# Kernel optimization log

Measured on AMD Instinct MI355X. Metric: run time of the kernel, lower is better.

## Reference

```python
import jax, jax.numpy as jnp
import numpy as np

D, H, N, T, B = 32, 128, 128, 256, 64   # input_dim, n_units, N_units, time_depth, batch
HEADS, THR, SHORT = 4, 0.01, 2
HD = H // HEADS


def setup_inputs() -> dict:
    key = jax.random.key(0)
    ks = iter(jax.random.split(key, 64))
    rn = lambda *s: jax.random.normal(next(ks), s, dtype=jnp.float32) * 0.1
    inp = {"x": jax.random.normal(next(ks), (B, T, D), dtype=jnp.float32)}
    for n_ in ["U_j", "U_i", "U_f", "U_o"]:
        inp[n_] = rn(D, 1, H)
    for n_ in ["W_j", "W_i", "W_f", "W_o"]:
        inp[n_] = rn(D, H, H)
    for n_ in ["B_j", "B_i", "B_f", "B_o"]:
        inp[n_] = jnp.full((D, H), 0.01, dtype=jnp.float32)
    for n_ in ["u_j", "u_i", "u_f", "u_o"]:
        inp[n_] = rn(D, N)
    for n_ in ["w_j", "w_i", "w_f", "w_o"]:
        inp[n_] = rn(N, N)
    for n_ in ["b_j", "b_i", "b_f", "b_o"]:
        inp[n_] = jnp.full((N,), 0.01, dtype=jnp.float32)
    inp["qkv_w"] = rn(3 * H, H)      # nn.Linear(H, 3H, bias=False) weight
    inp["out_w"] = rn(H, H)          # attn out_proj weight
    inp["h_proj_w"] = rn(N, H)       # nn.Linear(H, N, bias=False) weight
    inp["w_p"] = rn(N, 1)
    inp["b_p"] = jnp.zeros((1,), dtype=jnp.float32)
    return inp


def reference(x, U_j, U_i, U_f, U_o, W_j, W_i, W_f, W_o, B_j, B_i, B_f, B_o,
              u_j, u_i, u_f, u_o, w_j, w_i, w_f, w_o, b_j, b_i, b_f, b_o,
              qkv_w, out_w, h_proj_w, w_p, b_p):
    scale = 1.0 / jnp.sqrt(jnp.asarray(HD, dtype=x.dtype))

    def attention(h):  # h: (B, D, H) -> (B, D, H) cross-variable MHA
        qkv = h @ qkv_w.T                              # (B, D, 3H)
        q, k, v = jnp.split(qkv, 3, axis=-1)
        rs = lambda a: a.reshape(h.shape[0], D, HEADS, HD).transpose(0, 2, 1, 3)
        q, k, v = rs(q), rs(k), rs(v)                  # (B, heads, D, HD)
        scores = jnp.einsum('bhid,bhjd->bhij', q, k) * scale
        a = jax.nn.softmax(scores, axis=-1)
        a = jnp.where(a >= THR, a, jnp.zeros_like(a))
        ctx = jnp.einsum('bhij,bhjd->bhid', a, v)      # (B, heads, D, HD)
        ctx = ctx.transpose(0, 2, 1, 3).reshape(h.shape[0], D, H)
        return ctx @ out_w.T

    # per-variable input contributions: x_t[:, :, None] * U[:, 0, :]
    Uj, Ui, Uf, Uo = U_j[:, 0, :], U_i[:, 0, :], U_f[:, 0, :], U_o[:, 0, :]

    def step(carry, inputs):
        t, x_t = inputs                                # x_t: (B, D)
        h_var, c_var, h_mix, c_mix = carry
        xu = x_t[:, :, None]                            # (B, D, 1)
        j_var = jnp.tanh(jnp.einsum('bij,ijk->bik', h_var, W_j) + xu * Uj + B_j)
        i_var = jax.nn.sigmoid(jnp.einsum('bij,ijk->bik', h_var, W_i) + xu * Ui + B_i)
        f_var = jax.nn.sigmoid(jnp.einsum('bij,ijk->bik', h_var, W_f) + xu * Uf + B_f)
        o_var = jax.nn.sigmoid(jnp.einsum('bij,ijk->bik', h_var, W_o) + xu * Uo + B_o)
        c_var = c_var * f_var + i_var * j_var
        h_var = o_var * jnp.tanh(c_var)

        i_t = jax.nn.sigmoid(x_t @ u_i + h_mix @ w_i + b_i)
        f_t = jax.nn.sigmoid(x_t @ u_f + h_mix @ w_f + b_f)
        o_t = jax.nn.sigmoid(x_t @ u_o + h_mix @ w_o + b_o)
        j_t = jnp.tanh(x_t @ u_j + h_mix @ w_j + b_j)
        c_mix = f_t * c_mix + i_t * j_t
        h_mix_lstm = o_t * jnp.tanh(c_mix)

        z = attention(h_var)
        h_hat = z.mean(axis=1) @ h_proj_w.T            # (B, N)
        pred = h_hat @ w_p + b_p                       # (B, 1)
        h_mix = jnp.where(t > SHORT, h_hat, h_mix_lstm)
        return (h_var, c_var, h_mix, c_mix), pred

    z32 = jnp.zeros((x.shape[0], D, H), dtype=x.dtype)
    carry0 = (z32, z32,
              jnp.zeros((x.shape[0], N), dtype=x.dtype),
              jnp.zeros((x.shape[0], N), dtype=x.dtype))
    ts = jnp.arange(T - 1)
    xs = x.transpose(1, 0, 2)[: T - 1]                 # (T-1, B, D)
    _, preds = jax.lax.scan(step, carry0, (ts, xs))    # (T-1, B, 1)
    pred = preds[SHORT + 1:].transpose(1, 0, 2)        # (B, T-SHORT-2, 1)
    return pred
```

## Files before the change

### kernel.cpp

```cpp
#include <hip/hip_runtime.h>
#include <hip/hip_bf16.h>

typedef __hip_bfloat16 bf16;
typedef _Float16 f16x2 __attribute__((ext_vector_type(2)));
typedef _Float16 half8 __attribute__((ext_vector_type(8)));
typedef float f32x4 __attribute__((ext_vector_type(4)));

#define D_ 32
#define H_ 128
#define T_ 256
#define B_ 64
#define NSTEP 255
#define NOUT 252

#define F32_PROBE 0x3C23D70Au

#define MFMA_F16(A, B, C) __builtin_amdgcn_mfma_f32_16x16x32_f16(A, B, C, 0, 0, 0)

__device__ __forceinline__ float sigm(float v) {
    return __builtin_amdgcn_rcpf(1.0f + __expf(-v));
}
__device__ __forceinline__ float tanh_f(float x) {
    float xc = fminf(fmaxf(x, -9.0f), 9.0f);
    float e = __expf(-2.0f * xc);
    return (1.0f - e) * __builtin_amdgcn_rcpf(1.0f + e);
}

__device__ __forceinline__ unsigned int packh2(float a, float b) {
    union { unsigned int u; f16x2 h; } c;
    c.h[0] = (_Float16)a; c.h[1] = (_Float16)b;
    return c.u;
}
union U4H8 { uint4 u; half8 h; };
__device__ __forceinline__ half8 as_h8(uint4 u) { U4H8 x; x.u = u; return x.h; }

struct CvtArgs {
    const void* src[18];
    float* dst[18];
    int cnt[18];
    const unsigned int* probe;
};

__global__ __launch_bounds__(256) void k_convert(CvtArgs a)
{
    const bool isf32 = (*a.probe == F32_PROBE);
    const int seg = blockIdx.y;
    const int n = a.cnt[seg];
    const void* s = a.src[seg];
    float* dgt = a.dst[seg];
    for (int i = blockIdx.x * 256 + threadIdx.x; i < n; i += gridDim.x * 256) {
        float v;
        if (isf32) v = ((const float*)s)[i];
        else       v = __uint_as_float(((unsigned int)((const unsigned short*)s)[i]) << 16);
        dgt[i] = v;
    }
}

__global__ __launch_bounds__(256) void k_aux(
    const float* __restrict__ xf, float* __restrict__ xT,
    const float* __restrict__ qw, unsigned int* __restrict__ wpk,
    const float* __restrict__ hprj, const float* __restrict__ outw,
    const float* __restrict__ wp, const float* __restrict__ bp,
    float* __restrict__ vc)
{
    __shared__ float tile[64][33];
    const int bx = blockIdx.x;
    const int tid = threadIdx.x;

    if (bx < 256) {
        const int t = bx;
        for (int idx = tid; idx < 2048; idx += 256) {
            int b = idx >> 5, dd = idx & 31;
            tile[b][dd] = xf[((size_t)b * T_ + t) * D_ + dd];
        }
        __syncthreads();
        for (int idx = tid; idx < 2048; idx += 256) {
            int dd = idx >> 6, b = idx & 63;
            xT[((size_t)dd * T_ + t) * B_ + b] = tile[b][dd];
        }
    } else if (bx < 352) {
        int idx = (bx - 256) * 256 + tid;
        int e   = idx & 3;
        int w4  = idx >> 2;
        int l15 = w4 & 15;
        int l4  = (w4 >> 4) & 3;
        int ks  = (w4 >> 6) & 3;
        int mt  = w4 >> 8;
        int r   = mt * 16 + l15;
        int k2  = (ks * 4 + l4) * 4 + e;
        wpk[idx] = packh2(qw[r * 128 + 2 * k2], qw[r * 128 + 2 * k2 + 1]);
    } else {
        float* tmp = &tile[0][0];
        float s = 0.f;
        if (tid < 128) {
            for (int n = 0; n < 128; ++n) s += hprj[n * 128 + tid] * wp[n];
            tmp[tid] = s;
        }
        __syncthreads();
        if (tid < 128) {
            float v = 0.f;
            for (int c = 0; c < 128; ++c) v += outw[c * 128 + tid] * tmp[c];
            vc[tid] = v;
            if (tid == 0) vc[128] = bp[0];
        }
    }
}

__global__ __launch_bounds__(1024, 1) void k_recur(
    const float* __restrict__ xT, const float* __restrict__ wf,
    const float* __restrict__ uf, const float* __restrict__ bfv,
    float* __restrict__ cstg, unsigned int* __restrict__ h2g,
    unsigned int* __restrict__ hbw,
    int t0, int t1, int slots)
{
    __shared__ __align__(16) unsigned int hsw[2][512];
    __shared__ float xs[2048];

    const int tid  = threadIdx.x;
    const int lane = tid & 63;
    const int w    = tid >> 6;
    const int bx   = blockIdx.x;
    const int d    = bx >> 3;
    const int b0   = (bx & 7) * 8;
    const int l15  = lane & 15;
    const int l4   = lane >> 4;
    const int bb   = l15 & 7;
    const int sel  = l15 >> 3;

    const int ntot = (t1 - t0) * 8;
    for (int idx = tid; idx < ntot; idx += 1024) {
        int tr = idx >> 3, bbx = idx & 7;
        xs[idx] = xT[((size_t)d * T_ + (t0 + tr)) * B_ + b0 + bbx];
    }

    uint4 wfr[2][4];
    #pragma unroll
    for (int mtl = 0; mtl < 2; ++mtl) {
        const int c = w * 32 + mtl * 16 + l15;
        const int g = c & 3, h = c >> 2;
        const float* Wp = wf + (((size_t)g * 32 + d) * 128) * 128 + h;
        #pragma unroll
        for (int ks = 0; ks < 4; ++ks) {
            const int jb = ks * 32 + l4 * 8;
            uint4 u;
            u.x = packh2(Wp[(jb + 0) * 128], Wp[(jb + 1) * 128]);
            u.y = packh2(Wp[(jb + 2) * 128], Wp[(jb + 3) * 128]);
            u.z = packh2(Wp[(jb + 4) * 128], Wp[(jb + 5) * 128]);
            u.w = packh2(Wp[(jb + 6) * 128], Wp[(jb + 7) * 128]);
            wfr[mtl][ks] = u;
        }
    }
    float ur[2][4], br[2][4];
    #pragma unroll
    for (int mtl = 0; mtl < 2; ++mtl) {
        const int hq = w * 8 + mtl * 4 + l4;
        #pragma unroll
        for (int g = 0; g < 4; ++g) {
            ur[mtl][g] = uf [g * 4096 + d * H_ + hq];
            br[mtl][g] = bfv[g * 4096 + d * H_ + hq];
        }
    }

    float cs0;
    if (t0 == 0) cs0 = 0.f;
    else         cs0 = cstg[bx * 1024 + tid];

    {
        unsigned int* tgt = hsw[t0 & 1];
        if (t0 == 0) { if (tid < 512) tgt[tid] = 0u; }
        else         { if (tid < 512) tgt[tid] = h2g[bx * 512 + tid]; }
    }
    __syncthreads();

    const int wrd = sel * 2 + (l4 >> 1);
    const bool writer = !(l4 & 1);
    unsigned int pend = 0u;

    int sp = 0;
    { int t0m3 = t0 - 3; if (t0m3 > 0) sp = t0m3 % slots; }
    const size_t HSTRIDE = (size_t)B_ * 16 * 32 * 4;
    unsigned int* const hb0 =
        hbw + ((((size_t)b0 + bb) * 16 + w) * 32 + d) * 4 + wrd;
    unsigned int* hbp = hb0 + (size_t)sp * HSTRIDE;

    for (int t = t0; t < t1; ++t) {
        if (t > t0) {
            const int tp = t - 1;
            if (tp >= 3) {
                if (writer) *hbp = pend;
                ++sp; hbp += HSTRIDE;
                if (sp == slots) { sp = 0; hbp = hb0; }
            }
        }

        const unsigned int* hr = hsw[t & 1];
        unsigned int* hw       = hsw[(t & 1) ^ 1];

        uint4 hb[4];
        #pragma unroll
        for (int ks = 0; ks < 4; ++ks) {
            const int jc = ks * 4 + l4;
            hb[ks] = *(const uint4*)&hr[bb * 64 + (((jc ^ bb) & 15) << 2)];
        }
        const float xb = xs[(t - t0) * 8 + bb];

        f32x4 acc[2];
        #pragma unroll
        for (int mtl = 0; mtl < 2; ++mtl) {
            f32x4 a;
            a[0] = xb * ur[mtl][0] + br[mtl][0];
            a[1] = xb * ur[mtl][1] + br[mtl][1];
            a[2] = xb * ur[mtl][2] + br[mtl][2];
            a[3] = xb * ur[mtl][3] + br[mtl][3];
            acc[mtl] = a;
        }
        #pragma unroll
        for (int ks = 0; ks < 4; ++ks) {
            #pragma unroll
            for (int mtl = 0; mtl < 2; ++mtl)
                acc[mtl] = MFMA_F16(as_h8(wfr[mtl][ks]), as_h8(hb[ks]), acc[mtl]);
        }

        float a0 = sel ? acc[1][0] : acc[0][0];
        float a1 = sel ? acc[1][1] : acc[0][1];
        float a2 = sel ? acc[1][2] : acc[0][2];
        float a3 = sel ? acc[1][3] : acc[0][3];
        float jj = tanh_f(a0);
        float ii = sigm(a1);
        float ff = sigm(a2);
        float oo = sigm(a3);
        float cn = cs0 * ff + ii * jj;
        cs0 = cn;
        float hv = oo * tanh_f(cn);
        float pv = __shfl_xor(hv, 16);
        if (writer) {
            unsigned int hp = packh2(hv, pv);
            hw[bb * 64 + (((w ^ bb) & 15) << 2) + wrd] = hp;
            pend = hp;
        }
        __syncthreads();
    }

    {
        const int tp = t1 - 1;
        if (tp >= 3 && writer) *hbp = pend;
    }

    {
        const unsigned int* fin = hsw[t1 & 1];
        if (tid < 512) h2g[bx * 512 + tid] = fin[tid];
        cstg[bx * 1024 + tid] = cs0;
    }
}

#define QK_OFF  0
#define VT_OFF  16384
#define A_OFF   0
#define RED_OFF 24576
#define ATT_LDS 24640
#define TT_     4

__global__ __launch_bounds__(256, 2) void k_attn(
    const unsigned int* __restrict__ hbuf, const unsigned int* __restrict__ wpk,
    const float* __restrict__ vc, const unsigned int* __restrict__ probe,
    void* __restrict__ outv, int t0, int slots, int nt)
{
    __shared__ __align__(16) char S[ATT_LDS];

    const int tid  = threadIdx.x;
    const int lane = tid & 63;
    const int w    = tid >> 6;
    const int b    = blockIdx.y;
    const int tbase = t0 + TT_ * blockIdx.x;
    int ntt = nt - TT_ * (int)blockIdx.x;
    if (ntt > TT_) ntt = TT_;
    const int l15  = lane & 15;
    const int l4   = lane >> 4;

    uint4 wfr[6][4];
    #pragma unroll
    for (int mi = 0; mi < 6; ++mi) {
        #pragma unroll
        for (int ks = 0; ks < 4; ++ks)
            wfr[mi][ks] = ((const uint4*)wpk)[((w + 4 * mi) * 4 + ks) * 64 + lane];
    }
    const float vcr0 = vc[w * 32 + l15];
    const float vcr1 = vc[w * 32 + 16 + l15];

    const int s0 = (tbase - 3) % slots;
    const uint4* const hb4 = (const uint4*)hbuf;

    uint4 hfr[2][2][4];
    {
        const uint4* hp = hb4 + ((size_t)s0 * B_ + b) * 512;
        #pragma unroll
        for (int nt_ = 0; nt_ < 2; ++nt_)
            #pragma unroll
            for (int ks = 0; ks < 4; ++ks)
                hfr[0][nt_][ks] = hp[(ks * 4 + l4) * 32 + nt_ * 16 + l15];
    }

    #pragma unroll
    for (int tt = 0; tt < TT_; ++tt) {
        if (tt >= ntt) break;
        if (tt) __syncthreads();

        if (tt + 1 < ntt) {
            int sn = s0 + tt + 1; if (sn >= slots) sn -= slots;
            const uint4* hp = hb4 + ((size_t)sn * B_ + b) * 512;
            #pragma unroll
            for (int nt_ = 0; nt_ < 2; ++nt_)
                #pragma unroll
                for (int ks = 0; ks < 4; ++ks)
                    hfr[(tt + 1) & 1][nt_][ks] = hp[(ks * 4 + l4) * 32 + nt_ * 16 + l15];
        }

        #pragma unroll
        for (int mi = 0; mi < 6; ++mi) {
            const int mt  = w + 4 * mi;
            const int r0  = mt * 16 + (l4 << 2);
            const int tau = r0 >> 7;
            const int hd2 = (r0 >> 5) & 3;
            const int d0  = r0 & 31;
            #pragma unroll
            for (int nt_ = 0; nt_ < 2; ++nt_) {
                f32x4 acc = {0.f, 0.f, 0.f, 0.f};
                #pragma unroll
                for (int ks = 0; ks < 4; ++ks)
                    acc = MFMA_F16(as_h8(wfr[mi][ks]), as_h8(hfr[tt & 1][nt_][ks]), acc);
                const int ddc = nt_ * 16 + l15;
                if (tau < 2) {
                    unsigned int u0 = packh2(acc[0], acc[1]);
                    unsigned int u1 = packh2(acc[2], acc[3]);
                    const int c = (d0 >> 3) ^ ((ddc >> 1) & 3);
                    *(uint2*)(S + QK_OFF + (tau * 4 + hd2) * 2048 + ddc * 64
                              + c * 16 + ((2 * d0) & 15)) = make_uint2(u0, u1);
                } else {
                    #pragma unroll
                    for (int q = 0; q < 4; ++q) {
                        const int j = d0 + q;
                        const int c = (ddc >> 3) ^ ((j >> 1) & 3);
                        *(_Float16*)(S + VT_OFF + hd2 * 2048 + j * 64
                                     + c * 16 + ((2 * ddc) & 15)) = (_Float16)acc[q];
                    }
                }
            }
        }
        __syncthreads();

        uint4 qa[2], ka[2];
        #pragma unroll
        for (int It = 0; It < 2; ++It) {
            const int dd = It * 16 + l15;
            const int c = l4 ^ ((dd >> 1) & 3);
            qa[It] = *(const uint4*)(S + QK_OFF + (0 * 4 + w) * 2048 + dd * 64 + c * 16);
            ka[It] = *(const uint4*)(S + QK_OFF + (1 * 4 + w) * 2048 + dd * 64 + c * 16);
        }
        f32x4 st[2][2];
        #pragma unroll
        for (int Et = 0; Et < 2; ++Et)
            #pragma unroll
            for (int It = 0; It < 2; ++It) {
                f32x4 z = {0.f, 0.f, 0.f, 0.f};
                st[Et][It] = MFMA_F16(as_h8(ka[Et]), as_h8(qa[It]), z);
            }
        const float scale = 0.17677669529663687f;
        float mx[2], sum[2];
        #pragma unroll
        for (int It = 0; It < 2; ++It) {
            float m = -1e30f;
            #pragma unroll
            for (int Et = 0; Et < 2; ++Et)
                #pragma unroll
                for (int q = 0; q < 4; ++q) {
                    st[Et][It][q] *= scale;
                    m = fmaxf(m, st[Et][It][q]);
                }
            m = fmaxf(m, __shfl_xor(m, 16));
            m = fmaxf(m, __shfl_xor(m, 32));
            mx[It] = m;
        }
        #pragma unroll
        for (int It = 0; It < 2; ++It) {
            float s = 0.f;
            #pragma unroll
            for (int Et = 0; Et < 2; ++Et)
                #pragma unroll
                for (int q = 0; q < 4; ++q) {
                    float e = __expf(st[Et][It][q] - mx[It]);
                    st[Et][It][q] = e;
                    s += e;
                }
            s += __shfl_xor(s, 16);
            s += __shfl_xor(s, 32);
            sum[It] = s;
        }
        const float inv0 = 1.0f / sum[0];
        const float inv1 = 1.0f / sum[1];
        #pragma unroll
        for (int It = 0; It < 2; ++It) {
            const int i = It * 16 + l15;
            const float inv = It ? inv1 : inv0;
            #pragma unroll
            for (int Et = 0; Et < 2; ++Et)
                #pragma unroll
                for (int q = 0; q < 4; ++q) {
                    float a = st[Et][It][q] * inv;
                    if (a < 0.01f) a = 0.f;
                    const int e = Et * 16 + (l4 << 2) + q;
                    const int c = (e >> 3) ^ ((i >> 1) & 3);
                    *(_Float16*)(S + A_OFF + w * 2048 + i * 64
                                 + c * 16 + ((2 * e) & 15)) = (_Float16)a;
                }
        }
        uint4 aa[2], vb[2];
        #pragma unroll
        for (int It = 0; It < 2; ++It) {
            const int i = It * 16 + l15;
            const int c = l4 ^ ((i >> 1) & 3);
            aa[It] = *(const uint4*)(S + A_OFF + w * 2048 + i * 64 + c * 16);
        }
        #pragma unroll
        for (int Jt = 0; Jt < 2; ++Jt) {
            const int j = Jt * 16 + l15;
            const int c = l4 ^ ((j >> 1) & 3);
            vb[Jt] = *(const uint4*)(S + VT_OFF + w * 2048 + j * 64 + c * 16);
        }
        f32x4 ct[2][2];
        #pragma unroll
        for (int It = 0; It < 2; ++It)
            #pragma unroll
            for (int Jt = 0; Jt < 2; ++Jt) {
                f32x4 z = {0.f, 0.f, 0.f, 0.f};
                ct[It][Jt] = MFMA_F16(as_h8(aa[It]), as_h8(vb[Jt]), z);
            }
        float p = 0.f;
        #pragma unroll
        for (int Jt = 0; Jt < 2; ++Jt) {
            float cs_ = 0.f;
            #pragma unroll
            for (int It = 0; It < 2; ++It)
                #pragma unroll
                for (int q = 0; q < 4; ++q) cs_ += ct[It][Jt][q];
            cs_ += __shfl_xor(cs_, 16);
            cs_ += __shfl_xor(cs_, 32);
            p += cs_ * (Jt ? vcr1 : vcr0);
        }
        p *= (1.0f / 32.0f);
        p += __shfl_xor(p, 1);
        p += __shfl_xor(p, 2);
        p += __shfl_xor(p, 4);
        p += __shfl_xor(p, 8);
        if (lane == 0)
            *(float*)(S + RED_OFF + (tt * 4 + w) * 4) = p;
    }
    __syncthreads();

    if (tid < ntt) {
        const float* rd = (const float*)(S + RED_OFF);
        float r = rd[tid * 4] + rd[tid * 4 + 1] + rd[tid * 4 + 2] + rd[tid * 4 + 3]
                + vc[128];
        const int t = tbase + tid;
        size_t oidx = (size_t)b * NOUT + (t - 3);
        if (*probe == F32_PROBE) ((float*)outv)[oidx] = r;
        else                     ((bf16*)outv)[oidx]  = __float2bfloat16(r);
    }
}

extern "C" void kernel_launch(void* const* d_in, const int* in_sizes, int n_in,
                              void* d_out, int out_size, void* d_ws, size_t ws_size,
                              hipStream_t stream)
{
    float* ws = (float*)d_ws;
    float* xf    = ws;
    float* cstg  = ws;
    unsigned int* h2g = (unsigned int*)(ws + 262144);
    float* xT    = ws + 524288;
    float* wf    = ws + 1048576;
    float* uf    = ws + 3145728;
    float* bfv   = ws + 3162112;
    float* qkvwf = ws + 3178496;
    float* outwf = ws + 3227648;
    float* hprjf = ws + 3244032;
    float* wpf   = ws + 3260416;
    float* bpf   = ws + 3260544;
    float* vcomb = ws + 3260608;
    unsigned int* wpk = (unsigned int*)(ws + 3260800);
    unsigned short* hbuf = (unsigned short*)((char*)d_ws + 13141504);

    const unsigned int* probe = (const unsigned int*)d_in[9];

    CvtArgs ca;
    ca.src[0] = d_in[0];  ca.dst[0] = xf;  ca.cnt[0] = B_ * T_ * D_;
    for (int g = 0; g < 4; ++g) {
        ca.src[1 + g] = d_in[5 + g]; ca.dst[1 + g] = wf + (size_t)g * 524288; ca.cnt[1 + g] = 524288;
        ca.src[5 + g] = d_in[1 + g]; ca.dst[5 + g] = uf + g * 4096;           ca.cnt[5 + g] = 4096;
        ca.src[9 + g] = d_in[9 + g]; ca.dst[9 + g] = bfv + g * 4096;          ca.cnt[9 + g] = 4096;
    }
    ca.src[13] = d_in[25]; ca.dst[13] = qkvwf; ca.cnt[13] = 49152;
    ca.src[14] = d_in[26]; ca.dst[14] = outwf; ca.cnt[14] = 16384;
    ca.src[15] = d_in[27]; ca.dst[15] = hprjf; ca.cnt[15] = 16384;
    ca.src[16] = d_in[28]; ca.dst[16] = wpf;   ca.cnt[16] = 128;
    ca.src[17] = d_in[29]; ca.dst[17] = bpf;   ca.cnt[17] = 1;
    ca.probe = probe;

    k_convert<<<dim3(64, 18), dim3(256), 0, stream>>>(ca);
    k_aux<<<dim3(353), dim3(256), 0, stream>>>(
        xf, xT, qkvwf, wpk, hprjf, outwf, wpf, bpf, vcomb);

    long avail = (long)ws_size - 13141504L;
    int cap = (avail > 0) ? (int)(avail / 524288L) : 0;
    if (cap > NOUT) cap = NOUT;
    if (cap < 1) cap = 1;

    int t0c = 0;
    while (t0c < NSTEP) {
        int prod0 = (t0c < 3) ? 3 : t0c;
        int t1c = prod0 + cap;
        if (t1c > NSTEP) t1c = NSTEP;
        int nt = t1c - prod0;
        k_recur<<<dim3(256), dim3(1024), 0, stream>>>(
            xT, wf, uf, bfv, cstg, h2g, (unsigned int*)hbuf, t0c, t1c, cap);
        k_attn<<<dim3((nt + TT_ - 1) / TT_, 64), dim3(256), 0, stream>>>(
            (const unsigned int*)hbuf, wpk, vcomb, probe, d_out, prod0, cap, nt);
        t0c = t1c;
    }
}
```

Before: 430.9 us.

## Process attention timesteps in pairs with double LDS sets to halve barriers

Restructures the attention kernel's per-timestep loop so that two timesteps are handled per iteration, each writing its Q/K/V and attention matrices into its own LDS set. This halves the number of __syncthreads per block and gives the scheduler two independent softmax/MFMA chains to interleave. In exchange it drops the register prefetch of the next timestep's h fragments, doubles LDS usage to about 48KB per block, and raises register pressure, which may reduce occupancy under launch_bounds(256,2).

```diff
diff --git a/kernel.cpp b/kernel.cpp
--- a/kernel.cpp
+++ b/kernel.cpp
@@ -253,11 +253,10 @@
     }
 }
 
-#define QK_OFF  0
-#define VT_OFF  16384
-#define A_OFF   0
-#define RED_OFF 24576
-#define ATT_LDS 24640
+#define SET_SZ  24576
+#define VT_SOFF 16384
+#define RED_OFF 49152
+#define ATT_LDS 49216
 #define TT_     4
 
 __global__ __launch_bounds__(256, 2) void k_attn(
@@ -290,169 +289,179 @@
     const int s0 = (tbase - 3) % slots;
     const uint4* const hb4 = (const uint4*)hbuf;
 
-    uint4 hfr[2][2][4];
-    {
-        const uint4* hp = hb4 + ((size_t)s0 * B_ + b) * 512;
-        #pragma unroll
-        for (int nt_ = 0; nt_ < 2; ++nt_)
-            #pragma unroll
-            for (int ks = 0; ks < 4; ++ks)
-                hfr[0][nt_][ks] = hp[(ks * 4 + l4) * 32 + nt_ * 16 + l15];
-    }
-
-    #pragma unroll
-    for (int tt = 0; tt < TT_; ++tt) {
-        if (tt >= ntt) break;
-        if (tt) __syncthreads();
-
-        if (tt + 1 < ntt) {
-            int sn = s0 + tt + 1; if (sn >= slots) sn -= slots;
-            const uint4* hp = hb4 + ((size_t)sn * B_ + b) * 512;
-            #pragma unroll
-            for (int nt_ = 0; nt_ < 2; ++nt_)
-                #pragma unroll
-                for (int ks = 0; ks < 4; ++ks)
-                    hfr[(tt + 1) & 1][nt_][ks] = hp[(ks * 4 + l4) * 32 + nt_ * 16 + l15];
-        }
-
-        #pragma unroll
-        for (int mi = 0; mi < 6; ++mi) {
-            const int mt  = w + 4 * mi;
-            const int r0  = mt * 16 + (l4 << 2);
-            const int tau = r0 >> 7;
-            const int hd2 = (r0 >> 5) & 3;
-            const int d0  = r0 & 31;
-            #pragma unroll
-            for (int nt_ = 0; nt_ < 2; ++nt_) {
-                f32x4 acc = {0.f, 0.f, 0.f, 0.f};
-                #pragma unroll
-                for (int ks = 0; ks < 4; ++ks)
-                    acc = MFMA_F16(as_h8(wfr[mi][ks]), as_h8(hfr[tt & 1][nt_][ks]), acc);
-                const int ddc = nt_ * 16 + l15;
-                if (tau < 2) {
-                    unsigned int u0 = packh2(acc[0], acc[1]);
-                    unsigned int u1 = packh2(acc[2], acc[3]);
-                    const int c = (d0 >> 3) ^ ((ddc >> 1) & 3);
-                    *(uint2*)(S + QK_OFF + (tau * 4 + hd2) * 2048 + ddc * 64
-                              + c * 16 + ((2 * d0) & 15)) = make_uint2(u0, u1);
-                } else {
+    for (int tp = 0; tp < 2; ++tp) {
+        if (2 * tp >= ntt) break;
+        const int n2 = (ntt - 2 * tp >= 2) ? 2 : 1;
+        if (tp) __syncthreads();
+
+        #pragma unroll
+        for (int j = 0; j < 2; ++j) {
+            if (j < n2) {
+                int sl = s0 + 2 * tp + j; if (sl >= slots) sl -= slots;
+                const uint4* hp = hb4 + ((size_t)sl * B_ + b) * 512;
+                uint4 hfr[2][4];
+                #pragma unroll
+                for (int nt_ = 0; nt_ < 2; ++nt_)
+                    #pragma unroll
+                    for (int ks = 0; ks < 4; ++ks)
+                        hfr[nt_][ks] = hp[(ks * 4 + l4) * 32 + nt_ * 16 + l15];
+                char* SB = S + j * SET_SZ;
+                #pragma unroll
+                for (int mi = 0; mi < 6; ++mi) {
+                    const int mt  = w + 4 * mi;
+                    const int r0  = mt * 16 + (l4 << 2);
+                    const int tau = r0 >> 7;
+                    const int hd2 = (r0 >> 5) & 3;
+                    const int d0  = r0 & 31;
+                    #pragma unroll
+                    for (int nt_ = 0; nt_ < 2; ++nt_) {
+                        f32x4 acc = {0.f, 0.f, 0.f, 0.f};
+                        #pragma unroll
+                        for (int ks = 0; ks < 4; ++ks)
+                            acc = MFMA_F16(as_h8(wfr[mi][ks]), as_h8(hfr[nt_][ks]), acc);
+                        const int ddc = nt_ * 16 + l15;
+                        if (tau < 2) {
+                            unsigned int u0 = packh2(acc[0], acc[1]);
+                            unsigned int u1 = packh2(acc[2], acc[3]);
+                            const int c = (d0 >> 3) ^ ((ddc >> 1) & 3);
+                            *(uint2*)(SB + (tau * 4 + hd2) * 2048 + ddc * 64
+                                      + c * 16 + ((2 * d0) & 15)) = make_uint2(u0, u1);
+                        } else {
+                            #pragma unroll
+                            for (int q = 0; q < 4; ++q) {
+                                const int jv = d0 + q;
+                                const int c = (ddc >> 3) ^ ((jv >> 1) & 3);
+                                *(_Float16*)(SB + VT_SOFF + hd2 * 2048 + jv * 64
+                                             + c * 16 + ((2 * ddc) & 15)) = (_Float16)acc[q];
+                            }
+                        }
+                    }
+                }
+            }
+        }
+        __syncthreads();
+
+        uint4 qa[2][2], ka[2][2];
+        #pragma unroll
+        for (int j = 0; j < 2; ++j) if (j < n2) {
+            char* SB = S + j * SET_SZ;
+            #pragma unroll
+            for (int It = 0; It < 2; ++It) {
+                const int dd = It * 16 + l15;
+                const int c = l4 ^ ((dd >> 1) & 3);
+                qa[j][It] = *(const uint4*)(SB + (0 * 4 + w) * 2048 + dd * 64 + c * 16);
+                ka[j][It] = *(const uint4*)(SB + (1 * 4 + w) * 2048 + dd * 64 + c * 16);
+            }
+        }
+        f32x4 st[2][2][2];
+        #pragma unroll
+        for (int j = 0; j < 2; ++j) if (j < n2)
+            #pragma unroll
+            for (int Et = 0; Et < 2; ++Et)
+                #pragma unroll
+                for (int It = 0; It < 2; ++It) {
+                    f32x4 z = {0.f, 0.f, 0.f, 0.f};
+                    st[j][Et][It] = MFMA_F16(as_h8(ka[j][Et]), as_h8(qa[j][It]), z);
+                }
+        const float scale = 0.17677669529663687f;
+        float mx[2][2], sum[2][2];
+        #pragma unroll
+        for (int j = 0; j < 2; ++j) if (j < n2)
+            #pragma unroll
+            for (int It = 0; It < 2; ++It) {
+                float m = -1e30f;
+                #pragma unroll
+                for (int Et = 0; Et < 2; ++Et)
                     #pragma unroll
                     for (int q = 0; q < 4; ++q) {
-                        const int j = d0 + q;
-                        const int c = (ddc >> 3) ^ ((j >> 1) & 3);
-                        *(_Float16*)(S + VT_OFF + hd2 * 2048 + j * 64
-                                     + c * 16 + ((2 * ddc) & 15)) = (_Float16)acc[q];
+                        st[j][Et][It][q] *= scale;
+                        m = fmaxf(m, st[j][Et][It][q]);
                     }
+                m = fmaxf(m, __shfl_xor(m, 16));
+                m = fmaxf(m, __shfl_xor(m, 32));
+                mx[j][It] = m;
+            }
+        #pragma unroll
+        for (int j = 0; j < 2; ++j) if (j < n2)
+            #pragma unroll
+            for (int It = 0; It < 2; ++It) {
+                float s = 0.f;
+                #pragma unroll
+                for (int Et = 0; Et < 2; ++Et)
+                    #pragma unroll
+                    for (int q = 0; q < 4; ++q) {
+                        float e = __expf(st[j][Et][It][q] - mx[j][It]);
+                        st[j][Et][It][q] = e;
+                        s += e;
+                    }
+                s += __shfl_xor(s, 16);
+                s += __shfl_xor(s, 32);
+                sum[j][It] = s;
+            }
+        #pragma unroll
+        for (int j = 0; j < 2; ++j) if (j < n2) {
+            char* SB = S + j * SET_SZ;
+            #pragma unroll
+            for (int It = 0; It < 2; ++It) {
+                const int i = It * 16 + l15;
+                const float inv = 1.0f / sum[j][It];
+                #pragma unroll
+                for (int Et = 0; Et < 2; ++Et)
+                    #pragma unroll
+                    for (int q = 0; q < 4; ++q) {
+                        float a = st[j][Et][It][q] * inv;
+                        if (a < 0.01f) a = 0.f;
+                        const int e = Et * 16 + (l4 << 2) + q;
+                        const int c = (e >> 3) ^ ((i >> 1) & 3);
+                        *(_Float16*)(SB + w * 2048 + i * 64
+                                     + c * 16 + ((2 * e) & 15)) = (_Float16)a;
+                    }
+            }
+        }
+        #pragma unroll
+        for (int j = 0; j < 2; ++j) if (j < n2) {
+            char* SB = S + j * SET_SZ;
+            uint4 aa[2], vb[2];
+            #pragma unroll
+            for (int It = 0; It < 2; ++It) {
+                const int i = It * 16 + l15;
+                const int c = l4 ^ ((i >> 1) & 3);
+                aa[It] = *(const uint4*)(SB + w * 2048 + i * 64 + c * 16);
+            }
+            #pragma unroll
+            for (int Jt = 0; Jt < 2; ++Jt) {
+                const int jv = Jt * 16 + l15;
+                const int c = l4 ^ ((jv >> 1) & 3);
+                vb[Jt] = *(const uint4*)(SB + VT_SOFF + w * 2048 + jv * 64 + c * 16);
+            }
+            f32x4 ct[2][2];
+            #pragma unroll
+            for (int It = 0; It < 2; ++It)
+                #pragma unroll
+                for (int Jt = 0; Jt < 2; ++Jt) {
+                    f32x4 z = {0.f, 0.f, 0.f, 0.f};
+                    ct[It][Jt] = MFMA_F16(as_h8(aa[It]), as_h8(vb[Jt]), z);
                 }
-            }
-        }
-        __syncthreads();
-
-        uint4 qa[2], ka[2];
-        #pragma unroll
-        for (int It = 0; It < 2; ++It) {
-            const int dd = It * 16 + l15;
-            const int c = l4 ^ ((dd >> 1) & 3);
-            qa[It] = *(const uint4*)(S + QK_OFF + (0 * 4 + w) * 2048 + dd * 64 + c * 16);
-            ka[It] = *(const uint4*)(S + QK_OFF + (1 * 4 + w) * 2048 + dd * 64 + c * 16);
-        }
-        f32x4 st[2][2];
-        #pragma unroll
-        for (int Et = 0; Et < 2; ++Et)
-            #pragma unroll
-            for (int It = 0; It < 2; ++It) {
-                f32x4 z = {0.f, 0.f, 0.f, 0.f};
-                st[Et][It] = MFMA_F16(as_h8(ka[Et]), as_h8(qa[It]), z);
-            }
-        const float scale = 0.17677669529663687f;
-        float mx[2], sum[2];
-        #pragma unroll
-        for (int It = 0; It < 2; ++It) {
-            float m = -1e30f;
-            #pragma unroll
-            for (int Et = 0; Et < 2; ++Et)
-                #pragma unroll
-                for (int q = 0; q < 4; ++q) {
-                    st[Et][It][q] *= scale;
-                    m = fmaxf(m, st[Et][It][q]);
-                }
-            m = fmaxf(m, __shfl_xor(m, 16));
-            m = fmaxf(m, __shfl_xor(m, 32));
-            mx[It] = m;
-        }
-        #pragma unroll
-        for (int It = 0; It < 2; ++It) {
-            float s = 0.f;
-            #pragma unroll
-            for (int Et = 0; Et < 2; ++Et)
-                #pragma unroll
-                for (int q = 0; q < 4; ++q) {
-                    float e = __expf(st[Et][It][q] - mx[It]);
-                    st[Et][It][q] = e;
-                    s += e;
-                }
-            s += __shfl_xor(s, 16);
-            s += __shfl_xor(s, 32);
-            sum[It] = s;
-        }
-        const float inv0 = 1.0f / sum[0];
-        const float inv1 = 1.0f / sum[1];
-        #pragma unroll
-        for (int It = 0; It < 2; ++It) {
-            const int i = It * 16 + l15;
-            const float inv = It ? inv1 : inv0;
-            #pragma unroll
-            for (int Et = 0; Et < 2; ++Et)
-                #pragma unroll
-                for (int q = 0; q < 4; ++q) {
-                    float a = st[Et][It][q] * inv;
-                    if (a < 0.01f) a = 0.f;
-                    const int e = Et * 16 + (l4 << 2) + q;
-                    const int c = (e >> 3) ^ ((i >> 1) & 3);
-                    *(_Float16*)(S + A_OFF + w * 2048 + i * 64
-                                 + c * 16 + ((2 * e) & 15)) = (_Float16)a;
-                }
-        }
-        uint4 aa[2], vb[2];
-        #pragma unroll
-        for (int It = 0; It < 2; ++It) {
-            const int i = It * 16 + l15;
-            const int c = l4 ^ ((i >> 1) & 3);
-            aa[It] = *(const uint4*)(S + A_OFF + w * 2048 + i * 64 + c * 16);
-        }
-        #pragma unroll
-        for (int Jt = 0; Jt < 2; ++Jt) {
-            const int j = Jt * 16 + l15;
-            const int c = l4 ^ ((j >> 1) & 3);
-            vb[Jt] = *(const uint4*)(S + VT_OFF + w * 2048 + j * 64 + c * 16);
-        }
-        f32x4 ct[2][2];
-        #pragma unroll
-        for (int It = 0; It < 2; ++It)
+            float p = 0.f;
             #pragma unroll
             for (int Jt = 0; Jt < 2; ++Jt) {
-                f32x4 z = {0.f, 0.f, 0.f, 0.f};
-                ct[It][Jt] = MFMA_F16(as_h8(aa[It]), as_h8(vb[Jt]), z);
-            }
-        float p = 0.f;
-        #pragma unroll
-        for (int Jt = 0; Jt < 2; ++Jt) {
-            float cs_ = 0.f;
-            #pragma unroll
-            for (int It = 0; It < 2; ++It)
-                #pragma unroll
-                for (int q = 0; q < 4; ++q) cs_ += ct[It][Jt][q];
-            cs_ += __shfl_xor(cs_, 16);
-            cs_ += __shfl_xor(cs_, 32);
-            p += cs_ * (Jt ? vcr1 : vcr0);
-        }
-        p *= (1.0f / 32.0f);
-        p += __shfl_xor(p, 1);
-        p += __shfl_xor(p, 2);
-        p += __shfl_xor(p, 4);
-        p += __shfl_xor(p, 8);
-        if (lane == 0)
-            *(float*)(S + RED_OFF + (tt * 4 + w) * 4) = p;
+                float cs_ = 0.f;
+                #pragma unroll
+                for (int It = 0; It < 2; ++It)
+                    #pragma unroll
+                    for (int q = 0; q < 4; ++q) cs_ += ct[It][Jt][q];
+                cs_ += __shfl_xor(cs_, 16);
+                cs_ += __shfl_xor(cs_, 32);
+                p += cs_ * (Jt ? vcr1 : vcr0);
+            }
+            p *= (1.0f / 32.0f);
+            p += __shfl_xor(p, 1);
+            p += __shfl_xor(p, 2);
+            p += __shfl_xor(p, 4);
+            p += __shfl_xor(p, 8);
+            if (lane == 0)
+                *(float*)(S + RED_OFF + ((2 * tp + j) * 4 + w) * 4) = p;
+        }
     }
     __syncthreads();
 
```

After: 440.5 us. 1.02x slower.
